# Kernel optimization log

Measured on AMD Instinct MI355X. Metric: run time of the kernel, lower is better.

Reference implementation:

```python
import jax, jax.numpy as jnp
import numpy as np
from math import sqrt

N = 50000
E = 800000
D_EMB = 512
DK = 64
DV = 64
HEADS = 8


def setup_inputs() -> dict:
    key = jax.random.key(0)
    k1, k2, k3, k4 = jax.random.split(key, 4)
    x = jax.random.normal(k1, (N, D_EMB), dtype=jnp.float32)
    edge_index = jax.random.randint(k2, (2, E), 0, N, dtype=jnp.int64)
    out_qkv = (2 * DK + DV) * HEADS  # 1536
    W_qkv = jax.random.normal(k3, (out_qkv, D_EMB), dtype=jnp.float32) / sqrt(D_EMB)
    b_qkv = jnp.zeros((out_qkv,), dtype=jnp.float32)
    W_ff = jax.random.normal(k4, (D_EMB, DV * HEADS), dtype=jnp.float32) / sqrt(DV * HEADS)
    b_ff = jnp.zeros((D_EMB,), dtype=jnp.float32)
    return {"x": x, "edge_index": edge_index, "W_qkv": W_qkv, "b_qkv": b_qkv,
            "W_ff": W_ff, "b_ff": b_ff}


def _attention_message(Q, K, V, senders, receivers, n_nodes):
    # Q,K: [N, H, dK], V: [N, H, dV]; edge lists: [E]
    scale = 1.0 / sqrt(Q.shape[-1])
    # per-edge scores: [E, H]
    scores = jnp.einsum('ehd,ehd->eh', Q[receivers], K[senders]) * scale
    # segment softmax over incoming edges of each receiver
    smax = jax.ops.segment_max(scores, receivers, num_segments=n_nodes)  # [N, H]
    ex = jnp.exp(scores - smax[receivers])                               # [E, H]
    denom = jax.ops.segment_sum(ex, receivers, num_segments=n_nodes)    # [N, H]
    att = ex / denom[receivers]                                         # [E, H]
    # weighted scatter of V from senders to receivers: [N, H, dV]
    out = jax.ops.segment_sum(att[:, :, None] * V[senders], receivers,
                              num_segments=n_nodes)
    return out, att


def reference(x, edge_index, W_qkv, b_qkv, W_ff, b_ff):
    n_nodes = x.shape[0]
    qkv = x @ W_qkv.T + b_qkv  # [N, (2*dK+dV)*H]
    Q, K, V = jnp.split(qkv, [DK * HEADS, 2 * DK * HEADS], axis=-1)
    Q = Q.reshape(n_nodes, HEADS, DK)
    K = K.reshape(n_nodes, HEADS, DK)
    V = V.reshape(n_nodes, HEADS, DV)
    senders, receivers = edge_index[0], edge_index[1]
    msg, _ = _attention_message(Q, K, V, senders, receivers, n_nodes)
    # aggregate_heads: flatten heads and project to d_Embedding
    out = msg.reshape(n_nodes, HEADS * DV) @ W_ff.T + b_ff
    return out
```

## Files before the change

### kernel.cpp

```cpp
#include <hip/hip_runtime.h>

static constexpr int NN = 50000;
static constexpr int NE = 800000;
static constexpr int DEMB = 512;
static constexpr int QKV_OUT = 1536;

typedef _Float16 half8 __attribute__((ext_vector_type(8)));
typedef float floatx4 __attribute__((ext_vector_type(4)));

#define KQ_SCALE (127.0f / 5.5f)
#define KQ_DEQ   (5.5f / 127.0f)

static constexpr size_t OFF_QH   = 0;
static constexpr size_t OFF_K8   = 51200000;
static constexpr size_t OFF_V8   = 76800000;
static constexpr size_t OFF_MSG  = 102400000;
static constexpr size_t OFF_SRT  = 153600000;
static constexpr size_t OFF_DEG  = 156800000;
static constexpr size_t OFF_OFFA = 157000000;
static constexpr size_t OFF_CUR  = 157200064;
static constexpr size_t OFF_FLAG = 157400064;
static constexpr size_t OFF_WQH  = 157400128;
static constexpr size_t OFF_WFH  = 158972992;

typedef __attribute__((address_space(1))) const void* gas_ptr;
typedef __attribute__((address_space(3))) void* lds_ptr_t;

__device__ __forceinline__ void load_lds16(const void* g, void* l) {
  __builtin_amdgcn_global_load_lds((gas_ptr)g, (lds_ptr_t)l, 16, 0, 0);
}

__global__ __launch_bounds__(256)
void k_cvt(const float* __restrict__ in, _Float16* __restrict__ out, int n8) {
  int i = blockIdx.x * 256 + threadIdx.x;
  if (i < n8) {
    floatx4 a = *(const floatx4*)(in + (size_t)i * 8);
    floatx4 b = *(const floatx4*)(in + (size_t)i * 8 + 4);
    half8 h;
    #pragma unroll
    for (int q = 0; q < 4; ++q) { h[q] = (_Float16)a[q]; h[q + 4] = (_Float16)b[q]; }
    *(half8*)(out + (size_t)i * 8) = h;
  }
}

__global__ __launch_bounds__(64)
void k_detect64(const void* __restrict__ edge, int* __restrict__ flag) {
  if (threadIdx.x == 0) {
    const int* p = (const int*)edge;
    int is64 = 1;
    for (int i = 0; i < 16; ++i) if (p[2 * i + 1] != 0) is64 = 0;
    *flag = is64;
  }
}

__device__ __forceinline__ int edge_at(const void* edge, int row, int e, int is64) {
  if (is64) return (int)((const long long*)edge)[(size_t)row * NE + e];
  return ((const int*)edge)[(size_t)row * NE + e];
}

__global__ __launch_bounds__(256)
void k_histo(const void* __restrict__ edge, const int* __restrict__ flag,
             int* __restrict__ deg) {
  int e = blockIdx.x * 256 + threadIdx.x;
  if (e < NE) {
    int r = edge_at(edge, 1, e, *flag);
    atomicAdd(&deg[r], 1);
  }
}

__global__ __launch_bounds__(1024)
void k_scan(const int* __restrict__ deg, int* __restrict__ off,
            int* __restrict__ cur, int n) {
  __shared__ int sums[1024];
  int tid = threadIdx.x;
  int per = (n + 1023) >> 10;
  int start = tid * per;
  int end = start + per; if (end > n) end = n;
  int s = 0;
  for (int i = start; i < end; ++i) s += deg[i];
  sums[tid] = s;
  __syncthreads();
  for (int d = 1; d < 1024; d <<= 1) {
    int v = (tid >= d) ? sums[tid - d] : 0;
    __syncthreads();
    sums[tid] += v;
    __syncthreads();
  }
  int run = (tid == 0) ? 0 : sums[tid - 1];
  for (int i = start; i < end; ++i) {
    off[i] = run; cur[i] = run; run += deg[i];
  }
  if (tid == 0) off[n] = sums[1023];
}

__global__ __launch_bounds__(256)
void k_scatter(const void* __restrict__ edge, const int* __restrict__ flag,
               int* __restrict__ cur, int* __restrict__ srt) {
  int e = blockIdx.x * 256 + threadIdx.x;
  if (e < NE) {
    int is64 = *flag;
    int r = edge_at(edge, 1, e, is64);
    int s = edge_at(edge, 0, e, is64);
    int pos = atomicAdd(&cur[r], 1);
    srt[pos] = s;
  }
}

template<int MODE>
__global__ __launch_bounds__(512, 2)
void k_gemm256(const _Float16* __restrict__ Ah, const _Float16* __restrict__ Bh,
               const float* __restrict__ bias,
               void* __restrict__ out0, void* __restrict__ out1, void* __restrict__ out2,
               int M, int N, int K, int nxt) {
  __shared__ _Float16 lds[2][2][256 * 64];
  const int tid = threadIdx.x;

  const int nwg = gridDim.x;
  const int cpx = nwg >> 3;
  const int w = (blockIdx.x & 7) * cpx + (blockIdx.x >> 3);
  const int m0 = (w / nxt) * 256;
  const int n0 = (w % nxt) * 256;

  const int wid = tid >> 6, lane = tid & 63;
  const int wr = wid >> 2, wc = wid & 3;

  floatx4 acc[8][4];
  #pragma unroll
  for (int m = 0; m < 8; ++m)
    #pragma unroll
    for (int n = 0; n < 4; ++n)
      #pragma unroll
      for (int q = 0; q < 4; ++q) acc[m][n][q] = 0.f;

  const int srow = tid >> 3;
  const int sslot = tid & 7;
  const int scg = sslot ^ (srow & 7);

  int gar[4];
  #pragma unroll
  for (int c = 0; c < 4; ++c) {
    int gr = m0 + srow + c * 64;
    gar[c] = gr < M ? gr : M - 1;
  }
  const int gbr = n0 + srow;

  const int fr = lane & 15;
  const int fs = lane >> 4;

  const int KT = K >> 6;

  {
    _Float16* La = &lds[0][0][0];
    _Float16* Lb = &lds[0][1][0];
    #pragma unroll
    for (int c = 0; c < 4; ++c) {
      load_lds16(Ah + (size_t)gar[c] * K + scg * 8, (char*)La + c * 8192 + tid * 16);
      load_lds16(Bh + (size_t)(gbr + c * 64) * K + scg * 8, (char*)Lb + c * 8192 + tid * 16);
    }
  }
  __syncthreads();

  for (int t = 0; t < KT; ++t) {
    if (t + 1 < KT) {
      int k0 = (t + 1) << 6;
      _Float16* La = &lds[(t + 1) & 1][0][0];
      _Float16* Lb = &lds[(t + 1) & 1][1][0];
      #pragma unroll
      for (int c = 0; c < 4; ++c) {
        load_lds16(Ah + (size_t)gar[c] * K + k0 + scg * 8, (char*)La + c * 8192 + tid * 16);
        load_lds16(Bh + (size_t)(gbr + c * 64) * K + k0 + scg * 8, (char*)Lb + c * 8192 + tid * 16);
      }
    }
    const _Float16* La = &lds[t & 1][0][0];
    const _Float16* Lb = &lds[t & 1][1][0];
    #pragma unroll
    for (int kk = 0; kk < 2; ++kk) {
      half8 a[8], b[4];
      #pragma unroll
      for (int m = 0; m < 8; ++m) {
        int R = wr * 128 + m * 16 + fr;
        int s = (kk * 4 + fs) ^ (R & 7);
        a[m] = *(const half8*)(La + R * 64 + s * 8);
      }
      #pragma unroll
      for (int n = 0; n < 4; ++n) {
        int R = wc * 64 + n * 16 + fr;
        int s = (kk * 4 + fs) ^ (R & 7);
        b[n] = *(const half8*)(Lb + R * 64 + s * 8);
      }
      #pragma unroll
      for (int m = 0; m < 8; ++m)
        #pragma unroll
        for (int n = 0; n < 4; ++n)
          acc[m][n] = __builtin_amdgcn_mfma_f32_16x16x32_f16(a[m], b[n], acc[m][n], 0, 0, 0);
    }
    __syncthreads();
  }

  const int fq = fs << 2;
  #pragma unroll
  for (int m = 0; m < 8; ++m) {
    #pragma unroll
    for (int n = 0; n < 4; ++n) {
      int gn = n0 + wc * 64 + n * 16 + fr;
      float bv = bias[gn];
      #pragma unroll
      for (int q = 0; q < 4; ++q) {
        int gm = m0 + wr * 128 + m * 16 + fq + q;
        if (gm < M) {
          float val = acc[m][n][q] + bv;
          if (MODE == 0) {
            int region = gn >> 9;
            int col = gn & 511;
            size_t idx = (size_t)gm * 512 + col;
            if (region == 0) ((_Float16*)out0)[idx] = (_Float16)val;
            else {
              float s = fminf(fmaxf(val * KQ_SCALE, -127.f), 127.f);
              signed char c = (signed char)__float2int_rn(s);
              if (region == 1) ((signed char*)out1)[idx] = c;
              else             ((signed char*)out2)[idx] = c;
            }
          } else {
            ((float*)out0)[(size_t)gm * N + gn] = val;
          }
        }
      }
    }
  }
}

__global__ __launch_bounds__(256)
void k_attn(const _Float16* __restrict__ Qh, const signed char* __restrict__ K8,
            const signed char* __restrict__ V8, const int* __restrict__ off,
            const int* __restrict__ srt, _Float16* __restrict__ msg) {
  int r = blockIdx.x * 4 + (threadIdx.x >> 6);
  if (r >= NN) return;
  int lane = threadIdx.x & 63;
  int h = lane >> 3, j = lane & 7;
  int qoff = h * 64 + j * 8;

  half8 qh = *(const half8*)(Qh + (size_t)r * 512 + qoff);
  float q[8];
  #pragma unroll
  for (int i = 0; i < 8; ++i) q[i] = (float)qh[i] * 0.125f * KQ_DEQ;

  float denom = 0.f;
  float acc[8];
  #pragma unroll
  for (int i = 0; i < 8; ++i) acc[i] = 0.f;

  int e0 = off[r], e1 = off[r + 1];
  if (e1 <= e0) {
    half8 z = {};
    *(half8*)(msg + (size_t)r * 512 + qoff) = z;
    return;
  }

  auto gload = [&](uint2& k8, uint2& v8, int s) {
    k8 = *(const uint2*)(K8 + (size_t)s * 512 + qoff);
    v8 = *(const uint2*)(V8 + (size_t)s * 512 + qoff);
  };
  auto consume = [&](uint2 k8, uint2 v8) {
    int xw = (int)k8.x, yw = (int)k8.y;
    float p = 0.f;
    p += q[0] * (float)((xw << 24) >> 24);
    p += q[1] * (float)((xw << 16) >> 24);
    p += q[2] * (float)((xw << 8) >> 24);
    p += q[3] * (float)(xw >> 24);
    p += q[4] * (float)((yw << 24) >> 24);
    p += q[5] * (float)((yw << 16) >> 24);
    p += q[6] * (float)((yw << 8) >> 24);
    p += q[7] * (float)(yw >> 24);
    p += __shfl_xor(p, 1);
    p += __shfl_xor(p, 2);
    p += __shfl_xor(p, 4);
    float w = __expf(p);
    denom += w;
    int vx = (int)v8.x, vy = (int)v8.y;
    acc[0] += w * (float)((vx << 24) >> 24);
    acc[1] += w * (float)((vx << 16) >> 24);
    acc[2] += w * (float)((vx << 8) >> 24);
    acc[3] += w * (float)(vx >> 24);
    acc[4] += w * (float)((vy << 24) >> 24);
    acc[5] += w * (float)((vy << 16) >> 24);
    acc[6] += w * (float)((vy << 8) >> 24);
    acc[7] += w * (float)(vy >> 24);
  };
  auto sidx = [&](int e) { return srt[e < e1 ? e : e1 - 1]; };

  uint2 kb0, kb1, kb2, kb3, vb0, vb1, vb2, vb3;
  gload(kb0, vb0, sidx(e0));
  gload(kb1, vb1, sidx(e0 + 1));
  gload(kb2, vb2, sidx(e0 + 2));
  gload(kb3, vb3, sidx(e0 + 3));
  int sn0 = sidx(e0 + 4), sn1 = sidx(e0 + 5), sn2 = sidx(e0 + 6), sn3 = sidx(e0 + 7);

  int e = e0;
  for (; e + 4 <= e1; e += 4) {
    consume(kb0, vb0); gload(kb0, vb0, sn0);
    consume(kb1, vb1); gload(kb1, vb1, sn1);
    consume(kb2, vb2); gload(kb2, vb2, sn2);
    consume(kb3, vb3); gload(kb3, vb3, sn3);
    sn0 = sidx(e + 8); sn1 = sidx(e + 9); sn2 = sidx(e + 10); sn3 = sidx(e + 11);
  }
  int rem = e1 - e;
  if (rem > 0) consume(kb0, vb0);
  if (rem > 1) consume(kb1, vb1);
  if (rem > 2) consume(kb2, vb2);

  float inv = KQ_DEQ / denom;
  half8 oh;
  #pragma unroll
  for (int i = 0; i < 8; ++i) oh[i] = (_Float16)(acc[i] * inv);
  *(half8*)(msg + (size_t)r * 512 + qoff) = oh;
}

extern "C" void kernel_launch(void* const* d_in, const int* in_sizes, int n_in,
                              void* d_out, int out_size, void* d_ws, size_t ws_size,
                              hipStream_t stream) {
  const float* x     = (const float*)d_in[0];
  const void*  edge  = d_in[1];
  const float* W_qkv = (const float*)d_in[2];
  const float* b_qkv = (const float*)d_in[3];
  const float* W_ff  = (const float*)d_in[4];
  const float* b_ff  = (const float*)d_in[5];
  float* out = (float*)d_out;

  char* ws = (char*)d_ws;
  _Float16* Qh = (_Float16*)(ws + OFF_QH);
  signed char* K8 = (signed char*)(ws + OFF_K8);
  signed char* V8 = (signed char*)(ws + OFF_V8);
  _Float16* msgb = (_Float16*)(ws + OFF_MSG);
  _Float16* xh   = (_Float16*)(ws + OFF_MSG);
  int* srt  = (int*)(ws + OFF_SRT);
  int* deg  = (int*)(ws + OFF_DEG);
  int* offa = (int*)(ws + OFF_OFFA);
  int* cur  = (int*)(ws + OFF_CUR);
  int* flag = (int*)(ws + OFF_FLAG);
  _Float16* wqh = (_Float16*)(ws + OFF_WQH);
  _Float16* wfh = (_Float16*)(ws + OFF_WFH);

  hipMemsetAsync(deg, 0, NN * sizeof(int), stream);
  k_detect64<<<1, 64, 0, stream>>>(edge, flag);

  k_cvt<<<(NN * DEMB / 8 + 255) / 256, 256, 0, stream>>>(x, xh, NN * DEMB / 8);
  k_cvt<<<(QKV_OUT * DEMB / 8 + 255) / 256, 256, 0, stream>>>(W_qkv, wqh, QKV_OUT * DEMB / 8);
  k_cvt<<<(DEMB * DEMB / 8 + 255) / 256, 256, 0, stream>>>(W_ff, wfh, DEMB * DEMB / 8);

  k_gemm256<0><<<1176, 512, 0, stream>>>(
      xh, wqh, b_qkv, Qh, K8, V8, NN, QKV_OUT, DEMB, 6);

  k_histo<<<(NE + 255) / 256, 256, 0, stream>>>(edge, flag, deg);
  k_scan<<<1, 1024, 0, stream>>>(deg, offa, cur, NN);
  k_scatter<<<(NE + 255) / 256, 256, 0, stream>>>(edge, flag, cur, srt);

  k_attn<<<(NN + 3) / 4, 256, 0, stream>>>(Qh, K8, V8, offa, srt, msgb);

  k_gemm256<1><<<392, 512, 0, stream>>>(
      msgb, wfh, b_ff, out, nullptr, nullptr, NN, DEMB, DEMB, 2);
}
```

Baseline: 558.8 us.

## Split GEMM K-tile into half-stages with interleaved prefetch and MFMA priority

The GEMM's LDS tile is reorganised into two 32-wide K halves per buffer with a new XOR swizzle. Prefetching of the next tile is issued per half-stage, interleaved with the MFMA work on the current half. Explicit vmcnt waits plus barriers replace the single per-tile __syncthreads, and s_setprio raises wave priority around the MFMA block. The aim is finer-grained overlap of global-to-LDS loads with compute, at the cost of more barriers and some reliance on hand-counted vmcnt values.

```diff
diff --git a/kernel.cpp b/kernel.cpp
--- a/kernel.cpp
+++ b/kernel.cpp
@@ -112,7 +112,7 @@
                const float* __restrict__ bias,
                void* __restrict__ out0, void* __restrict__ out1, void* __restrict__ out2,
                int M, int N, int K, int nxt) {
-  __shared__ _Float16 lds[2][2][256 * 64];
+  __shared__ _Float16 lds[2][2][2][256 * 32];
   const int tid = threadIdx.x;
 
   const int nwg = gridDim.x;
@@ -132,69 +132,66 @@
       #pragma unroll
       for (int q = 0; q < 4; ++q) acc[m][n][q] = 0.f;
 
-  const int srow = tid >> 3;
-  const int sslot = tid & 7;
-  const int scg = sslot ^ (srow & 7);
-
-  int gar[4];
-  #pragma unroll
-  for (int c = 0; c < 4; ++c) {
-    int gr = m0 + srow + c * 64;
-    gar[c] = gr < M ? gr : M - 1;
-  }
-  const int gbr = n0 + srow;
+  const int srow = tid >> 2;
+  const int schunk = (tid & 3) ^ ((tid >> 3) & 3);
+  int garow[2];
+  #pragma unroll
+  for (int c = 0; c < 2; ++c) {
+    int gr = m0 + c * 128 + srow;
+    garow[c] = gr < M ? gr : M - 1;
+  }
+  const int gbrow0 = n0 + srow, gbrow1 = n0 + 128 + srow;
 
   const int fr = lane & 15;
   const int fs = lane >> 4;
 
   const int KT = K >> 6;
 
-  {
-    _Float16* La = &lds[0][0][0];
-    _Float16* Lb = &lds[0][1][0];
-    #pragma unroll
-    for (int c = 0; c < 4; ++c) {
-      load_lds16(Ah + (size_t)gar[c] * K + scg * 8, (char*)La + c * 8192 + tid * 16);
-      load_lds16(Bh + (size_t)(gbr + c * 64) * K + scg * 8, (char*)Lb + c * 8192 + tid * 16);
-    }
-  }
+  auto STAGE = [&](int tt, int kk) {
+    const size_t kbase = (size_t)tt * 64 + kk * 32 + schunk * 8;
+    char* La = (char*)&lds[tt & 1][kk][0][0];
+    char* Lb = (char*)&lds[tt & 1][kk][1][0];
+    load_lds16(Ah + (size_t)garow[0] * K + kbase, La + tid * 16);
+    load_lds16(Ah + (size_t)garow[1] * K + kbase, La + 8192 + tid * 16);
+    load_lds16(Bh + (size_t)gbrow0 * K + kbase, Lb + tid * 16);
+    load_lds16(Bh + (size_t)gbrow1 * K + kbase, Lb + 8192 + tid * 16);
+  };
+
+  STAGE(0, 0);
+  STAGE(0, 1);
   __syncthreads();
 
   for (int t = 0; t < KT; ++t) {
-    if (t + 1 < KT) {
-      int k0 = (t + 1) << 6;
-      _Float16* La = &lds[(t + 1) & 1][0][0];
-      _Float16* Lb = &lds[(t + 1) & 1][1][0];
-      #pragma unroll
-      for (int c = 0; c < 4; ++c) {
-        load_lds16(Ah + (size_t)gar[c] * K + k0 + scg * 8, (char*)La + c * 8192 + tid * 16);
-        load_lds16(Bh + (size_t)(gbr + c * 64) * K + k0 + scg * 8, (char*)Lb + c * 8192 + tid * 16);
-      }
-    }
-    const _Float16* La = &lds[t & 1][0][0];
-    const _Float16* Lb = &lds[t & 1][1][0];
+    const bool st = (t + 1 < KT);
     #pragma unroll
     for (int kk = 0; kk < 2; ++kk) {
+      if (st) STAGE(t + 1, kk);
+      const _Float16* La = &lds[t & 1][kk][0][0];
+      const _Float16* Lb = &lds[t & 1][kk][1][0];
       half8 a[8], b[4];
       #pragma unroll
       for (int m = 0; m < 8; ++m) {
         int R = wr * 128 + m * 16 + fr;
-        int s = (kk * 4 + fs) ^ (R & 7);
-        a[m] = *(const half8*)(La + R * 64 + s * 8);
+        int s = fs ^ ((R >> 1) & 3);
+        a[m] = *(const half8*)(La + R * 32 + s * 8);
       }
       #pragma unroll
       for (int n = 0; n < 4; ++n) {
         int R = wc * 64 + n * 16 + fr;
-        int s = (kk * 4 + fs) ^ (R & 7);
-        b[n] = *(const half8*)(Lb + R * 64 + s * 8);
+        int s = fs ^ ((R >> 1) & 3);
+        b[n] = *(const half8*)(Lb + R * 32 + s * 8);
       }
+      __builtin_amdgcn_s_setprio(1);
       #pragma unroll
       for (int m = 0; m < 8; ++m)
         #pragma unroll
         for (int n = 0; n < 4; ++n)
           acc[m][n] = __builtin_amdgcn_mfma_f32_16x16x32_f16(a[m], b[n], acc[m][n], 0, 0, 0);
+      __builtin_amdgcn_s_setprio(0);
+      if (st) asm volatile("s_waitcnt vmcnt(4)" ::: "memory");
+      else    asm volatile("s_waitcnt vmcnt(0)" ::: "memory");
+      __builtin_amdgcn_s_barrier();
     }
-    __syncthreads();
   }
 
   const int fq = fs << 2;
```

New measurement: 605.8 us. 1.08x slower.
